# Kernel tuning notes

Hardware: AMD Instinct MI355X
Metric: run time of the kernel (lower is better)

Reference implementation:

```python
import jax, jax.numpy as jnp
import numpy as np

N = 100000   # nodes
E = 640000   # edges
F = 128      # num_features
D = 128      # dim
G = 128      # graphs in batch
BN_EPS = 1e-5


def setup_inputs() -> dict:
    key = jax.random.key(0)
    ks = jax.random.split(key, 16)
    lin = lambda k, i, o: (jax.random.normal(k, (i, o), jnp.float32) / np.sqrt(i)).astype(jnp.float32)
    inp = {
        "x": jax.random.normal(ks[0], (N, F), jnp.float32),
        "edge_index": jax.random.randint(ks[1], (2, E), 0, N),
        "batch": jnp.sort(jax.random.randint(ks[2], (N,), 0, G)),
        # layer 0: Linear(F,D)-ReLU-Linear(D,D), BN(D)
        "W0a": lin(ks[3], F, D), "b0a": jnp.zeros((D,), jnp.float32),
        "W0b": lin(ks[4], D, D), "b0b": jnp.zeros((D,), jnp.float32),
        "g0": jnp.ones((D,), jnp.float32), "be0": jnp.zeros((D,), jnp.float32),
        # layer 1: Linear(D,D)-ReLU-Linear(D,D), BN(D)
        "W1a": lin(ks[5], D, D), "b1a": jnp.zeros((D,), jnp.float32),
        "W1b": lin(ks[6], D, D), "b1b": jnp.zeros((D,), jnp.float32),
        "g1": jnp.ones((D,), jnp.float32), "be1": jnp.zeros((D,), jnp.float32),
        # layer 2: Linear(D,D)-ReLU-Linear(D,1), BN(1)
        "W2a": lin(ks[7], D, D), "b2a": jnp.zeros((D,), jnp.float32),
        "W2b": lin(ks[8], D, 1), "b2b": jnp.zeros((1,), jnp.float32),
        "g2": jnp.ones((1,), jnp.float32), "be2": jnp.zeros((1,), jnp.float32),
    }
    return inp


def _gin_layer(x, src, dst, Wa, ba, Wb, bb, g, be, relu_out):
    # GINConv (eps=0): h = x + sum_{j in N(i)} x_j, then MLP, then BN (train-mode stats)
    agg = jax.ops.segment_sum(x[src], dst, num_segments=N)
    h = x + agg
    h = jax.nn.relu(h @ Wa + ba) @ Wb + bb
    mu = jnp.mean(h, axis=0)
    var = jnp.mean((h - mu) ** 2, axis=0)  # biased var (torch BN normalization)
    h = (h - mu) * jax.lax.rsqrt(var + BN_EPS) * g + be
    return jax.nn.relu(h) if relu_out else h


def reference(x, edge_index, batch,
              W0a, b0a, W0b, b0b, g0, be0,
              W1a, b1a, W1b, b1b, g1, be1,
              W2a, b2a, W2b, b2b, g2, be2):
    src, dst = edge_index[0], edge_index[1]
    h = _gin_layer(x, src, dst, W0a, b0a, W0b, b0b, g0, be0, True)
    h = _gin_layer(h, src, dst, W1a, b1a, W1b, b1b, g1, be1, True)
    h = _gin_layer(h, src, dst, W2a, b2a, W2b, b2b, g2, be2, False)  # [N,1], no final ReLU
    # segment softmax over graphs, temperature 5.0 (PyG softmax semantics)
    z = h / 5.0
    m = jax.ops.segment_max(z, batch, num_segments=G)
    ez = jnp.exp(z - m[batch])
    s = jax.ops.segment_sum(ez, batch, num_segments=G)
    return ez / (s[batch] + 1e-16)
```

## Files before the change

kernel.cpp:

```cpp
#include <hip/hip_runtime.h>
#include <math.h>

#define NN 100000
#define EE 640000
#define GG 128
#define BN_EPS 1e-5f
#define NBLK 98

typedef __attribute__((ext_vector_type(8))) short short8;
typedef __attribute__((ext_vector_type(4))) float f32x4;


__device__ __forceinline__ short f2bf(float f) {
    unsigned u = __float_as_uint(f);
    u += 0x7fffu + ((u >> 16) & 1);
    return (short)(u >> 16);
}
__device__ __forceinline__ float bf2f(short s) {
    return __uint_as_float(((unsigned)(unsigned short)s) << 16);
}
__device__ __forceinline__ int swz(int row, int chunk) {
    return row * 128 + ((chunk ^ (row & 15)) << 3);
}
__device__ __forceinline__ int swze(int row, int col) {
    return row * 128 + (((col >> 3) ^ (row & 15)) << 3) + (col & 7);
}

__global__ void k_setup(const float* __restrict__ W0a, const float* __restrict__ W0b,
                        const float* __restrict__ W1a, const float* __restrict__ W1b,
                        const float* __restrict__ W2a, short* __restrict__ Wt,
                        int* __restrict__ deg, float* __restrict__ smf) {
    int idx = blockIdx.x * 256 + threadIdx.x;
    if (idx < 81920) {
        int wi = idx >> 14, r = idx & 16383;
        const float* W = (wi == 0) ? W0a : (wi == 1) ? W0b : (wi == 2) ? W1a
                        : (wi == 3) ? W1b : W2a;
        int k = r >> 7, n = r & 127;
        Wt[wi * 16384 + n * 128 + k] = f2bf(W[k * 128 + n]);
    }
    if (idx < NN) deg[idx] = 0;
    if (idx < 4112) smf[idx] = 0.0f;
}

__global__ void k_hist(const int* __restrict__ ei, int* __restrict__ deg) {
    int e = blockIdx.x * 256 + threadIdx.x;
    if (e < EE) atomicAdd(&deg[ei[EE + e]], 1);
}

__global__ __launch_bounds__(1024) void k_scan1(const int* __restrict__ deg,
                                                int* __restrict__ offs,
                                                int* __restrict__ bsums) {
    __shared__ int sm[1024];
    int t = threadIdx.x;
    int i = blockIdx.x * 1024 + t;
    int v = (i < NN) ? deg[i] : 0;
    sm[t] = v;
    __syncthreads();
    for (int off = 1; off < 1024; off <<= 1) {
        int add = (t >= off) ? sm[t - off] : 0;
        __syncthreads();
        sm[t] += add;
        __syncthreads();
    }
    if (i < NN) offs[i] = sm[t] - v;
    if (t == 1023) bsums[blockIdx.x] = sm[1023];
}

__global__ void k_scan2(int* bsums) {
    __shared__ int sm[128];
    int t = threadIdx.x;
    int v = (t < NBLK) ? bsums[t] : 0;
    sm[t] = v;
    __syncthreads();
    for (int off = 1; off < 128; off <<= 1) {
        int add = (t >= off) ? sm[t - off] : 0;
        __syncthreads();
        sm[t] += add;
        __syncthreads();
    }
    if (t < NBLK) bsums[t] = sm[t] - v;
}

__global__ __launch_bounds__(1024) void k_scan3(int* __restrict__ offs,
                                                const int* __restrict__ bsums,
                                                int* __restrict__ pos) {
    int t = threadIdx.x;
    int i = blockIdx.x * 1024 + t;
    if (i < NN) {
        int o = offs[i] + bsums[blockIdx.x];
        offs[i] = o;
        pos[i] = o;
    }
    if (i == 0) offs[NN] = EE;
}

__global__ void k_fill(const int* __restrict__ ei, int* __restrict__ pos,
                       int* __restrict__ csr) {
    int e = blockIdx.x * 256 + threadIdx.x;
    if (e < EE) {
        int d = ei[EE + e];
        int p = atomicAdd(&pos[d], 1);
        csr[p] = ei[e];
    }
}

__global__ void k_gather0(const float* __restrict__ x, const int* __restrict__ offs,
                          const int* __restrict__ csr, short* __restrict__ agg) {
    int tt = blockIdx.x * 256 + threadIdx.x;
    int n = tt >> 4, l = tt & 15;
    if (n >= NN) return;
    int j0 = offs[n], j1 = offs[n + 1];
    const float4* xr = (const float4*)(x + (size_t)n * 128) + l * 2;
    float4 a0 = xr[0], a1 = xr[1];
    float f[8] = {a0.x, a0.y, a0.z, a0.w, a1.x, a1.y, a1.z, a1.w};
    for (int j = j0; j < j1; ++j) {
        int s = csr[j];
        const float4* sr = (const float4*)(x + (size_t)s * 128) + l * 2;
        float4 b0 = sr[0], b1 = sr[1];
        f[0] += b0.x; f[1] += b0.y; f[2] += b0.z; f[3] += b0.w;
        f[4] += b1.x; f[5] += b1.y; f[6] += b1.z; f[7] += b1.w;
    }
    short8 o;
#pragma unroll
    for (int j = 0; j < 8; ++j) o[j] = f2bf(f[j]);
    *(short8*)(agg + (size_t)n * 128 + l * 8) = o;
}

__global__ void k_gatherb(const short* __restrict__ h, const int* __restrict__ offs,
                          const int* __restrict__ csr, const float* __restrict__ rep,
                          const float* __restrict__ g, const float* __restrict__ be,
                          short* __restrict__ agg) {
    __shared__ float parS[128], parH[128];
    int t = threadIdx.x;
    if (t < 128) {
        float s = 0.f, ss = 0.f;
#pragma unroll
        for (int r = 0; r < 8; ++r) {
            s += rep[r * 256 + t];
            ss += rep[r * 256 + 128 + t];
        }
        const float inv = 1.0f / (float)NN;
        float mu = s * inv;
        float var = ss * inv - mu * mu;
        float sc = g[t] / sqrtf(var + BN_EPS);
        parS[t] = sc;
        parH[t] = be[t] - mu * sc;
    }
    __syncthreads();
    int tt = blockIdx.x * 256 + t;
    int n = tt >> 4, l = tt & 15;
    if (n >= NN) return;
    float sc[8], sh[8];
#pragma unroll
    for (int j = 0; j < 8; ++j) { sc[j] = parS[l * 8 + j]; sh[j] = parH[l * 8 + j]; }
    int j0 = offs[n], j1 = offs[n + 1];
    short8 v = *(const short8*)(h + (size_t)n * 128 + l * 8);
    float f[8];
#pragma unroll
    for (int j = 0; j < 8; ++j) f[j] = fmaxf(fmaf(bf2f(v[j]), sc[j], sh[j]), 0.f);
    for (int j = j0; j < j1; ++j) {
        int s = csr[j];
        short8 w = *(const short8*)(h + (size_t)s * 128 + l * 8);
#pragma unroll
        for (int k = 0; k < 8; ++k) f[k] += fmaxf(fmaf(bf2f(w[k]), sc[k], sh[k]), 0.f);
    }
    short8 o;
#pragma unroll
    for (int j = 0; j < 8; ++j) o[j] = f2bf(f[j]);
    *(short8*)(agg + (size_t)n * 128 + l * 8) = o;
}

template <bool SECOND>
__global__ __launch_bounds__(256, 2) void k_mlp(const short* __restrict__ hin,
                                                const short* __restrict__ Wta,
                                                const float* __restrict__ ba,
                                                const short* __restrict__ Wtb,
                                                const float* __restrict__ bb,
                                                short* __restrict__ hout,
                                                float* __restrict__ statsRep,
                                                const float* __restrict__ w2,
                                                const float* __restrict__ b2,
                                                float* __restrict__ z,
                                                float* __restrict__ s2rep) {
    __shared__ short Asb[16384];
    __shared__ short Wsb[16384];
    const int t = threadIdx.x;
    const int row0 = blockIdx.x * 128;
    const int lane = t & 63, wave = t >> 6;
    const int r16 = lane & 15, q = lane >> 4;
    const int rh = wave & 1, ch = wave >> 1;
    const int RA = rh * 64, CB = ch * 64;

    short8 wpre[8];
#pragma unroll
    for (int i = 0; i < 8; ++i) {
        int f = i * 256 + t;
        int r = f >> 4, c8 = f & 15;
        int gr = row0 + r;
        short8 v = {0, 0, 0, 0, 0, 0, 0, 0};
        if (gr < NN) v = *(const short8*)(hin + (size_t)gr * 128 + c8 * 8);
        *(short8*)&Asb[swz(r, c8)] = v;
        *(short8*)&Wsb[swz(r, c8)] = *(const short8*)(Wta + r * 128 + c8 * 8);
        if constexpr (SECOND) wpre[i] = *(const short8*)(Wtb + r * 128 + c8 * 8);
    }
    __syncthreads();

    f32x4 acc[4][4];
#pragma unroll
    for (int rt = 0; rt < 4; ++rt)
#pragma unroll
        for (int ct = 0; ct < 4; ++ct) acc[rt][ct] = (f32x4)0.f;

#pragma unroll
    for (int kk = 0; kk < 4; ++kk) {
        short8 b[4], a[4];
#pragma unroll
        for (int ct = 0; ct < 4; ++ct)
            b[ct] = *(const short8*)&Wsb[swz(CB + ct * 16 + r16, kk * 4 + q)];
#pragma unroll
        for (int rt = 0; rt < 4; ++rt)
            a[rt] = *(const short8*)&Asb[swz(RA + rt * 16 + r16, kk * 4 + q)];
#pragma unroll
        for (int rt = 0; rt < 4; ++rt)
#pragma unroll
            for (int ct = 0; ct < 4; ++ct)
                acc[rt][ct] = __builtin_amdgcn_mfma_f32_16x16x32_bf16(a[rt], b[ct], acc[rt][ct], 0, 0, 0);
    }
    __syncthreads();

    float bav[4];
#pragma unroll
    for (int ct = 0; ct < 4; ++ct) bav[ct] = ba[CB + ct * 16 + r16];
#pragma unroll
    for (int rt = 0; rt < 4; ++rt)
#pragma unroll
        for (int ct = 0; ct < 4; ++ct)
#pragma unroll
            for (int rg = 0; rg < 4; ++rg) {
                float m = fmaxf(acc[rt][ct][rg] + bav[ct], 0.f);
                Asb[swze(RA + rt * 16 + q * 4 + rg, CB + ct * 16 + r16)] = f2bf(m);
            }

    if constexpr (!SECOND) {
        __syncthreads();
        const int l16 = t & 15, rr = t >> 4;
        float4 w0 = ((const float4*)w2)[l16 * 2];
        float4 w1 = ((const float4*)w2)[l16 * 2 + 1];
        float b2v = b2[0];
        float s = 0.f, ss = 0.f;
#pragma unroll
        for (int pass = 0; pass < 8; ++pass) {
            int r = pass * 16 + rr;
            int gr = row0 + r;
            short8 v = *(const short8*)&Asb[swz(r, l16)];
            float p = bf2f(v[0]) * w0.x + bf2f(v[1]) * w0.y + bf2f(v[2]) * w0.z +
                      bf2f(v[3]) * w0.w + bf2f(v[4]) * w1.x + bf2f(v[5]) * w1.y +
                      bf2f(v[6]) * w1.z + bf2f(v[7]) * w1.w;
#pragma unroll
            for (int off = 1; off < 16; off <<= 1) p += __shfl_xor(p, off, 16);
            if (l16 == 0 && gr < NN) {
                float h2 = p + b2v;
                z[gr] = h2;
                s += h2;
                ss += h2 * h2;
            }
        }
        s += __shfl_xor(s, 16); s += __shfl_xor(s, 32);
        ss += __shfl_xor(ss, 16); ss += __shfl_xor(ss, 32);
        float* rsm = (float*)Wsb;
        if ((t & 63) == 0) { rsm[wave * 2] = s; rsm[wave * 2 + 1] = ss; }
        __syncthreads();
        if (t == 0) {
            float S = rsm[0] + rsm[2] + rsm[4] + rsm[6];
            float SS = rsm[1] + rsm[3] + rsm[5] + rsm[7];
            int rp = (blockIdx.x & 7) * 2;
            unsafeAtomicAdd(&s2rep[rp], S);
            unsafeAtomicAdd(&s2rep[rp + 1], SS);
        }
        return;
    } else {
#pragma unroll
        for (int i = 0; i < 8; ++i) {
            int f = i * 256 + t;
            int r = f >> 4, c8 = f & 15;
            *(short8*)&Wsb[swz(r, c8)] = wpre[i];
        }
        __syncthreads();

#pragma unroll
        for (int rt = 0; rt < 4; ++rt)
#pragma unroll
            for (int ct = 0; ct < 4; ++ct) acc[rt][ct] = (f32x4)0.f;

#pragma unroll
        for (int kk = 0; kk < 4; ++kk) {
            short8 b[4], a[4];
#pragma unroll
            for (int ct = 0; ct < 4; ++ct)
                b[ct] = *(const short8*)&Wsb[swz(CB + ct * 16 + r16, kk * 4 + q)];
#pragma unroll
            for (int rt = 0; rt < 4; ++rt)
                a[rt] = *(const short8*)&Asb[swz(RA + rt * 16 + r16, kk * 4 + q)];
#pragma unroll
            for (int rt = 0; rt < 4; ++rt)
#pragma unroll
                for (int ct = 0; ct < 4; ++ct)
                    acc[rt][ct] = __builtin_amdgcn_mfma_f32_16x16x32_bf16(a[rt], b[ct], acc[rt][ct], 0, 0, 0);
        }
        __syncthreads();

        float bbv[4];
#pragma unroll
        for (int ct = 0; ct < 4; ++ct) bbv[ct] = bb[CB + ct * 16 + r16];
        float s[4] = {0.f, 0.f, 0.f, 0.f}, ss[4] = {0.f, 0.f, 0.f, 0.f};
#pragma unroll
        for (int rt = 0; rt < 4; ++rt)
#pragma unroll
            for (int ct = 0; ct < 4; ++ct)
#pragma unroll
                for (int rg = 0; rg < 4; ++rg) {
                    int lr = RA + rt * 16 + q * 4 + rg;
                    int gr = row0 + lr;
                    float hv = acc[rt][ct][rg] + bbv[ct];
                    if (gr < NN) { s[ct] += hv; ss[ct] += hv * hv; }
                    Asb[swze(lr, CB + ct * 16 + r16)] = f2bf(hv);
                }
#pragma unroll
        for (int ct = 0; ct < 4; ++ct) {
            s[ct] += __shfl_xor(s[ct], 16);
            s[ct] += __shfl_xor(s[ct], 32);
            ss[ct] += __shfl_xor(ss[ct], 16);
            ss[ct] += __shfl_xor(ss[ct], 32);
        }
        float* redF = (float*)Wsb;
        if (lane < 16) {
#pragma unroll
            for (int ct = 0; ct < 4; ++ct) {
                int col = CB + ct * 16 + r16;
                redF[rh * 256 + col] = s[ct];
                redF[rh * 256 + 128 + col] = ss[ct];
            }
        }
        __syncthreads();
        {
            float v = redF[t] + redF[256 + t];
            unsafeAtomicAdd(&statsRep[(blockIdx.x & 7) * 256 + t], v);
        }
#pragma unroll
        for (int i = 0; i < 8; ++i) {
            int f = i * 256 + t;
            int r = f >> 4, c8 = f & 15;
            int gr = row0 + r;
            if (gr < NN)
                *(short8*)(hout + (size_t)gr * 128 + c8 * 8) = *(const short8*)&Asb[swz(r, c8)];
        }
    }
}

__device__ __forceinline__ int lbound(const int* __restrict__ b, int val) {
    int lo = 0, hi = NN;
    while (lo < hi) {
        int m = (lo + hi) >> 1;
        if (b[m] < val) lo = m + 1; else hi = m;
    }
    return lo;
}

__global__ void k_softmax(const float* __restrict__ zr, const float* __restrict__ s2rep,
                          const float* __restrict__ g2, const float* __restrict__ be2,
                          const int* __restrict__ batch, float* __restrict__ out) {
    __shared__ float rb[4];
    const int g = blockIdx.x, t = threadIdx.x;
    const int lo = lbound(batch, g), hi = lbound(batch, g + 1);
    float s = 0.f, ssq = 0.f;
#pragma unroll
    for (int i = 0; i < 8; ++i) { s += s2rep[i * 2]; ssq += s2rep[i * 2 + 1]; }
    const float mu = s / (float)NN;
    const float var = ssq / (float)NN - mu * mu;
    const float sc = g2[0] / sqrtf(var + BN_EPS) * 0.2f;
    const float sh = (be2[0] - mu * g2[0] / sqrtf(var + BN_EPS)) * 0.2f;

    float m = -INFINITY;
    for (int i = lo + t; i < hi; i += 256) m = fmaxf(m, fmaf(zr[i], sc, sh));
#pragma unroll
    for (int off = 1; off < 64; off <<= 1) m = fmaxf(m, __shfl_xor(m, off, 64));
    if ((t & 63) == 0) rb[t >> 6] = m;
    __syncthreads();
    float gmax = fmaxf(fmaxf(rb[0], rb[1]), fmaxf(rb[2], rb[3]));
    __syncthreads();

    float sum = 0.f;
    for (int i = lo + t; i < hi; i += 256) {
        float e = expf(fmaf(zr[i], sc, sh) - gmax);
        out[i] = e;
        sum += e;
    }
#pragma unroll
    for (int off = 1; off < 64; off <<= 1) sum += __shfl_xor(sum, off, 64);
    if ((t & 63) == 0) rb[t >> 6] = sum;
    __syncthreads();
    float S = rb[0] + rb[1] + rb[2] + rb[3];
    float inv = 1.0f / (S + 1e-16f);
    for (int i = lo + t; i < hi; i += 256) out[i] *= inv;
}

extern "C" void kernel_launch(void* const* d_in, const int* in_sizes, int n_in,
                              void* d_out, int out_size, void* d_ws, size_t ws_size,
                              hipStream_t stream) {
    const float* x   = (const float*)d_in[0];
    const int* ei    = (const int*)d_in[1];
    const int* batch = (const int*)d_in[2];
    const float *W0a = (const float*)d_in[3],  *b0a = (const float*)d_in[4];
    const float *W0b = (const float*)d_in[5],  *b0b = (const float*)d_in[6];
    const float *g0  = (const float*)d_in[7],  *be0 = (const float*)d_in[8];
    const float *W1a = (const float*)d_in[9],  *b1a = (const float*)d_in[10];
    const float *W1b = (const float*)d_in[11], *b1b = (const float*)d_in[12];
    const float *g1  = (const float*)d_in[13], *be1 = (const float*)d_in[14];
    const float *W2a = (const float*)d_in[15], *b2a = (const float*)d_in[16];
    const float *W2b = (const float*)d_in[17], *b2b = (const float*)d_in[18];
    const float *g2  = (const float*)d_in[19], *be2 = (const float*)d_in[20];
    float* out = (float*)d_out;

    char* wsb = (char*)d_ws;
    short* Abf = (short*)wsb;
    short* Bbf = (short*)(wsb + 25600000);
    float* Zb  = (float*)(wsb + 51200000);
    float* SMf = (float*)(wsb + 51600000);
    float* S0r = SMf;
    float* S1r = SMf + 2048;
    float* S2r = SMf + 4096;
    int* offs  = (int*)(wsb + 51620000);
    int* bsums = (int*)(wsb + 52020004);
    int* csr   = (int*)(wsb + 52020516);
    short* Wt  = (short*)(wsb + 54580544);
    int* deg = (int*)wsb;
    int* pos = (int*)(wsb + 400000);

    const int gE   = (EE + 255) / 256;
    const int gG16 = (NN * 16) / 256;
    const int gMlp = (NN + 127) / 128;

    k_setup<<<391, 256, 0, stream>>>(W0a, W0b, W1a, W1b, W2a, Wt, deg, SMf);

    k_hist<<<gE, 256, 0, stream>>>(ei, deg);
    k_scan1<<<NBLK, 1024, 0, stream>>>(deg, offs, bsums);
    k_scan2<<<1, 128, 0, stream>>>(bsums);
    k_scan3<<<NBLK, 1024, 0, stream>>>(offs, bsums, pos);
    k_fill<<<gE, 256, 0, stream>>>(ei, pos, csr);

    k_gather0<<<gG16, 256, 0, stream>>>(x, offs, csr, Abf);
    k_mlp<true><<<gMlp, 256, 0, stream>>>(Abf, Wt, b0a, Wt + 16384, b0b, Abf, S0r,
                                          nullptr, nullptr, nullptr, nullptr);
    k_gatherb<<<gG16, 256, 0, stream>>>(Abf, offs, csr, S0r, g0, be0, Bbf);
    k_mlp<true><<<gMlp, 256, 0, stream>>>(Bbf, Wt + 2 * 16384, b1a, Wt + 3 * 16384, b1b,
                                          Bbf, S1r, nullptr, nullptr, nullptr, nullptr);
    k_gatherb<<<gG16, 256, 0, stream>>>(Bbf, offs, csr, S1r, g1, be1, Abf);
    k_mlp<false><<<gMlp, 256, 0, stream>>>(Abf, Wt + 4 * 16384, b2a, nullptr, nullptr,
                                           nullptr, nullptr, W2b, b2b, Zb, S2r);

    k_softmax<<<GG, 256, 0, stream>>>(Zb, S2r, g2, be2, batch, out);
}
```

Measured before the change: 401.1 us.

## Fuse neighbor aggregation into MLP kernels and precompute BN params separately

The separate gather kernels are removed. Neighbor aggregation (with BN+ReLU of the previous layer applied on the fly) now happens inside the MLP kernel while it fills the LDS A tile, so the bf16 aggregate no longer goes through global memory. BN scale and shift are now computed once by a small k_bnpar kernel instead of in every gather block, and the neighbor loop prefetches the next row. The trade-off is that the irregular gather latency now sits inside a kernel limited to 2 blocks per CU by its launch bounds, so there may be less latency hiding than the standalone gather kernels had.

```diff
diff --git a/kernel.cpp b/kernel.cpp
--- a/kernel.cpp
+++ b/kernel.cpp
@@ -104,74 +104,28 @@
     }
 }
 
-__global__ void k_gather0(const float* __restrict__ x, const int* __restrict__ offs,
-                          const int* __restrict__ csr, short* __restrict__ agg) {
-    int tt = blockIdx.x * 256 + threadIdx.x;
-    int n = tt >> 4, l = tt & 15;
-    if (n >= NN) return;
-    int j0 = offs[n], j1 = offs[n + 1];
-    const float4* xr = (const float4*)(x + (size_t)n * 128) + l * 2;
-    float4 a0 = xr[0], a1 = xr[1];
-    float f[8] = {a0.x, a0.y, a0.z, a0.w, a1.x, a1.y, a1.z, a1.w};
-    for (int j = j0; j < j1; ++j) {
-        int s = csr[j];
-        const float4* sr = (const float4*)(x + (size_t)s * 128) + l * 2;
-        float4 b0 = sr[0], b1 = sr[1];
-        f[0] += b0.x; f[1] += b0.y; f[2] += b0.z; f[3] += b0.w;
-        f[4] += b1.x; f[5] += b1.y; f[6] += b1.z; f[7] += b1.w;
-    }
-    short8 o;
-#pragma unroll
-    for (int j = 0; j < 8; ++j) o[j] = f2bf(f[j]);
-    *(short8*)(agg + (size_t)n * 128 + l * 8) = o;
-}
-
-__global__ void k_gatherb(const short* __restrict__ h, const int* __restrict__ offs,
-                          const int* __restrict__ csr, const float* __restrict__ rep,
-                          const float* __restrict__ g, const float* __restrict__ be,
-                          short* __restrict__ agg) {
-    __shared__ float parS[128], parH[128];
-    int t = threadIdx.x;
-    if (t < 128) {
-        float s = 0.f, ss = 0.f;
-#pragma unroll
-        for (int r = 0; r < 8; ++r) {
-            s += rep[r * 256 + t];
-            ss += rep[r * 256 + 128 + t];
-        }
-        const float inv = 1.0f / (float)NN;
-        float mu = s * inv;
-        float var = ss * inv - mu * mu;
-        float sc = g[t] / sqrtf(var + BN_EPS);
-        parS[t] = sc;
-        parH[t] = be[t] - mu * sc;
-    }
-    __syncthreads();
-    int tt = blockIdx.x * 256 + t;
-    int n = tt >> 4, l = tt & 15;
-    if (n >= NN) return;
-    float sc[8], sh[8];
-#pragma unroll
-    for (int j = 0; j < 8; ++j) { sc[j] = parS[l * 8 + j]; sh[j] = parH[l * 8 + j]; }
-    int j0 = offs[n], j1 = offs[n + 1];
-    short8 v = *(const short8*)(h + (size_t)n * 128 + l * 8);
-    float f[8];
-#pragma unroll
-    for (int j = 0; j < 8; ++j) f[j] = fmaxf(fmaf(bf2f(v[j]), sc[j], sh[j]), 0.f);
-    for (int j = j0; j < j1; ++j) {
-        int s = csr[j];
-        short8 w = *(const short8*)(h + (size_t)s * 128 + l * 8);
-#pragma unroll
-        for (int k = 0; k < 8; ++k) f[k] += fmaxf(fmaf(bf2f(w[k]), sc[k], sh[k]), 0.f);
-    }
-    short8 o;
-#pragma unroll
-    for (int j = 0; j < 8; ++j) o[j] = f2bf(f[j]);
-    *(short8*)(agg + (size_t)n * 128 + l * 8) = o;
-}
-
-template <bool SECOND>
-__global__ __launch_bounds__(256, 2) void k_mlp(const short* __restrict__ hin,
+__global__ void k_bnpar(const float* __restrict__ rep, const float* __restrict__ g,
+                        const float* __restrict__ be, float* __restrict__ par) {
+    int c = threadIdx.x;
+    float s = 0.f, ss = 0.f;
+#pragma unroll
+    for (int r = 0; r < 8; ++r) {
+        s += rep[r * 256 + c];
+        ss += rep[r * 256 + 128 + c];
+    }
+    const float inv = 1.0f / (float)NN;
+    float mu = s * inv;
+    float var = ss * inv - mu * mu;
+    float sc = g[c] / sqrtf(var + BN_EPS);
+    par[c] = sc;
+    par[128 + c] = be[c] - mu * sc;
+}
+
+template <int MODE>
+__global__ __launch_bounds__(256, 2) void k_mlp(const void* __restrict__ hin_,
+                                                const int* __restrict__ offs,
+                                                const int* __restrict__ csr,
+                                                const float* __restrict__ par,
                                                 const short* __restrict__ Wta,
                                                 const float* __restrict__ ba,
                                                 const short* __restrict__ Wtb,
@@ -190,18 +144,84 @@
     const int r16 = lane & 15, q = lane >> 4;
     const int rh = wave & 1, ch = wave >> 1;
     const int RA = rh * 64, CB = ch * 64;
+    const int c8 = t & 15;
+    const int rbase = t >> 4;
+
+    float sc[8], sh[8];
+    if constexpr (MODE != 0) {
+        const float4* ps = (const float4*)par + c8 * 2;
+        float4 s0 = ps[0], s1 = ps[1];
+        const float4* ph = (const float4*)(par + 128) + c8 * 2;
+        float4 h0 = ph[0], h1 = ph[1];
+        sc[0] = s0.x; sc[1] = s0.y; sc[2] = s0.z; sc[3] = s0.w;
+        sc[4] = s1.x; sc[5] = s1.y; sc[6] = s1.z; sc[7] = s1.w;
+        sh[0] = h0.x; sh[1] = h0.y; sh[2] = h0.z; sh[3] = h0.w;
+        sh[4] = h1.x; sh[5] = h1.y; sh[6] = h1.z; sh[7] = h1.w;
+    }
 
     short8 wpre[8];
 #pragma unroll
     for (int i = 0; i < 8; ++i) {
-        int f = i * 256 + t;
-        int r = f >> 4, c8 = f & 15;
+        int r = i * 16 + rbase;
+        *(short8*)&Wsb[swz(r, c8)] = *(const short8*)(Wta + r * 128 + c8 * 8);
+        if constexpr (MODE != 2) wpre[i] = *(const short8*)(Wtb + r * 128 + c8 * 8);
+    }
+
+#pragma unroll
+    for (int i = 0; i < 8; ++i) {
+        int r = i * 16 + rbase;
         int gr = row0 + r;
-        short8 v = {0, 0, 0, 0, 0, 0, 0, 0};
-        if (gr < NN) v = *(const short8*)(hin + (size_t)gr * 128 + c8 * 8);
-        *(short8*)&Asb[swz(r, c8)] = v;
-        *(short8*)&Wsb[swz(r, c8)] = *(const short8*)(Wta + r * 128 + c8 * 8);
-        if constexpr (SECOND) wpre[i] = *(const short8*)(Wtb + r * 128 + c8 * 8);
+        float a8[8] = {0.f, 0.f, 0.f, 0.f, 0.f, 0.f, 0.f, 0.f};
+        if (gr < NN) {
+            int j0 = offs[gr], j1 = offs[gr + 1];
+            if constexpr (MODE == 0) {
+                const float* xp = (const float*)hin_;
+                const float4* xr = (const float4*)(xp + (size_t)gr * 128) + c8 * 2;
+                float4 v0 = xr[0], v1 = xr[1];
+                a8[0] = v0.x; a8[1] = v0.y; a8[2] = v0.z; a8[3] = v0.w;
+                a8[4] = v1.x; a8[5] = v1.y; a8[6] = v1.z; a8[7] = v1.w;
+                if (j0 < j1) {
+                    int s = csr[j0];
+                    const float4* sr = (const float4*)(xp + (size_t)s * 128) + c8 * 2;
+                    float4 w0 = sr[0], w1 = sr[1];
+                    for (int j = j0 + 1; j < j1; ++j) {
+                        int s2 = csr[j];
+                        const float4* nr = (const float4*)(xp + (size_t)s2 * 128) + c8 * 2;
+                        float4 n0 = nr[0], n1 = nr[1];
+                        a8[0] += w0.x; a8[1] += w0.y; a8[2] += w0.z; a8[3] += w0.w;
+                        a8[4] += w1.x; a8[5] += w1.y; a8[6] += w1.z; a8[7] += w1.w;
+                        w0 = n0; w1 = n1;
+                    }
+                    a8[0] += w0.x; a8[1] += w0.y; a8[2] += w0.z; a8[3] += w0.w;
+                    a8[4] += w1.x; a8[5] += w1.y; a8[6] += w1.z; a8[7] += w1.w;
+                }
+            } else {
+                const short* hp = (const short*)hin_;
+                short8 v = *(const short8*)(hp + (size_t)gr * 128 + c8 * 8);
+#pragma unroll
+                for (int k = 0; k < 8; ++k)
+                    a8[k] = fmaxf(fmaf(bf2f(v[k]), sc[k], sh[k]), 0.f);
+                if (j0 < j1) {
+                    int s = csr[j0];
+                    short8 w = *(const short8*)(hp + (size_t)s * 128 + c8 * 8);
+                    for (int j = j0 + 1; j < j1; ++j) {
+                        int s2 = csr[j];
+                        short8 n = *(const short8*)(hp + (size_t)s2 * 128 + c8 * 8);
+#pragma unroll
+                        for (int k = 0; k < 8; ++k)
+                            a8[k] += fmaxf(fmaf(bf2f(w[k]), sc[k], sh[k]), 0.f);
+                        w = n;
+                    }
+#pragma unroll
+                    for (int k = 0; k < 8; ++k)
+                        a8[k] += fmaxf(fmaf(bf2f(w[k]), sc[k], sh[k]), 0.f);
+                }
+            }
+        }
+        short8 o;
+#pragma unroll
+        for (int k = 0; k < 8; ++k) o[k] = f2bf(a8[k]);
+        *(short8*)&Asb[swz(r, c8)] = o;
     }
     __syncthreads();
 
@@ -241,7 +261,7 @@
                 Asb[swze(RA + rt * 16 + q * 4 + rg, CB + ct * 16 + r16)] = f2bf(m);
             }
 
-    if constexpr (!SECOND) {
+    if constexpr (MODE == 2) {
         __syncthreads();
         const int l16 = t & 15, rr = t >> 4;
         float4 w0 = ((const float4*)w2)[l16 * 2];
@@ -281,8 +301,7 @@
     } else {
 #pragma unroll
         for (int i = 0; i < 8; ++i) {
-            int f = i * 256 + t;
-            int r = f >> 4, c8 = f & 15;
+            int r = i * 16 + rbase;
             *(short8*)&Wsb[swz(r, c8)] = wpre[i];
         }
         __syncthreads();
@@ -348,8 +367,7 @@
         }
 #pragma unroll
         for (int i = 0; i < 8; ++i) {
-            int f = i * 256 + t;
-            int r = f >> 4, c8 = f & 15;
+            int r = i * 16 + rbase;
             int gr = row0 + r;
             if (gr < NN)
                 *(short8*)(hout + (size_t)gr * 128 + c8 * 8) = *(const short8*)&Asb[swz(r, c8)];
@@ -429,6 +447,8 @@
     float* S0r = SMf;
     float* S1r = SMf + 2048;
     float* S2r = SMf + 4096;
+    float* P0  = SMf + 4112;
+    float* P1  = SMf + 4368;
     int* offs  = (int*)(wsb + 51620000);
     int* bsums = (int*)(wsb + 52020004);
     int* csr   = (int*)(wsb + 52020516);
@@ -437,7 +457,6 @@
     int* pos = (int*)(wsb + 400000);
 
     const int gE   = (EE + 255) / 256;
-    const int gG16 = (NN * 16) / 256;
     const int gMlp = (NN + 127) / 128;
 
     k_setup<<<391, 256, 0, stream>>>(W0a, W0b, W1a, W1b, W2a, Wt, deg, SMf);
@@ -448,15 +467,17 @@
     k_scan3<<<NBLK, 1024, 0, stream>>>(offs, bsums, pos);
     k_fill<<<gE, 256, 0, stream>>>(ei, pos, csr);
 
-    k_gather0<<<gG16, 256, 0, stream>>>(x, offs, csr, Abf);
-    k_mlp<true><<<gMlp, 256, 0, stream>>>(Abf, Wt, b0a, Wt + 16384, b0b, Abf, S0r,
-                                          nullptr, nullptr, nullptr, nullptr);
-    k_gatherb<<<gG16, 256, 0, stream>>>(Abf, offs, csr, S0r, g0, be0, Bbf);
-    k_mlp<true><<<gMlp, 256, 0, stream>>>(Bbf, Wt + 2 * 16384, b1a, Wt + 3 * 16384, b1b,
-                                          Bbf, S1r, nullptr, nullptr, nullptr, nullptr);
-    k_gatherb<<<gG16, 256, 0, stream>>>(Bbf, offs, csr, S1r, g1, be1, Abf);
-    k_mlp<false><<<gMlp, 256, 0, stream>>>(Abf, Wt + 4 * 16384, b2a, nullptr, nullptr,
-                                           nullptr, nullptr, W2b, b2b, Zb, S2r);
+    k_mlp<0><<<gMlp, 256, 0, stream>>>(x, offs, csr, nullptr,
+                                       Wt, b0a, Wt + 16384, b0b, Abf, S0r,
+                                       nullptr, nullptr, nullptr, nullptr);
+    k_bnpar<<<1, 128, 0, stream>>>(S0r, g0, be0, P0);
+    k_mlp<1><<<gMlp, 256, 0, stream>>>(Abf, offs, csr, P0,
+                                       Wt + 2 * 16384, b1a, Wt + 3 * 16384, b1b, Bbf, S1r,
+                                       nullptr, nullptr, nullptr, nullptr);
+    k_bnpar<<<1, 128, 0, stream>>>(S1r, g1, be1, P1);
+    k_mlp<2><<<gMlp, 256, 0, stream>>>(Bbf, offs, csr, P1,
+                                       Wt + 4 * 16384, b2a, nullptr, nullptr, nullptr, nullptr,
+                                       W2b, b2b, Zb, S2r);
 
     k_softmax<<<GG, 256, 0, stream>>>(Zb, S2r, g2, be2, batch, out);
 }
```

Measured after the change: 463.5 us. +15.6%, slower.
